# Kernel optimization log

Hardware: AMD Instinct MI355X
Metric: run time of the kernel (lower is better)

## Reference

```python
import math
import jax, jax.numpy as jnp
import numpy as np

L, W, H, T, B = 12, 1024, 16, 1024, 2
CH = W // H  # per-head channels
SCALE = 1.0 / math.sqrt(math.sqrt(CH))
STD = 0.25 * math.sqrt(1.0 / W)  # init_scale * sqrt(1/width)


def setup_inputs() -> dict:
    key = jax.random.key(0)
    ks = jax.random.split(key, 8)
    x = jax.random.normal(ks[0], (B, T, W), dtype=jnp.float32)
    qkv_w = jax.random.normal(ks[1], (L, W, 3 * W), dtype=jnp.float32) * STD
    qkv_b = jnp.zeros((L, 3 * W), jnp.float32)
    proj_w = jax.random.normal(ks[2], (L, W, W), dtype=jnp.float32) * STD
    proj_b = jnp.zeros((L, W), jnp.float32)
    ln1_g = jnp.ones((L, W), jnp.float32)
    ln1_b = jnp.zeros((L, W), jnp.float32)
    ln2_g = jnp.ones((L, W), jnp.float32)
    ln2_b = jnp.zeros((L, W), jnp.float32)
    fc_w = jax.random.normal(ks[3], (L, W, 4 * W), dtype=jnp.float32) * STD
    fc_b = jnp.zeros((L, 4 * W), jnp.float32)
    fc2_w = jax.random.normal(ks[4], (L, 4 * W, W), dtype=jnp.float32) * STD
    fc2_b = jnp.zeros((L, W), jnp.float32)
    return dict(x=x, qkv_w=qkv_w, qkv_b=qkv_b, proj_w=proj_w, proj_b=proj_b,
                ln1_g=ln1_g, ln1_b=ln1_b, ln2_g=ln2_g, ln2_b=ln2_b,
                fc_w=fc_w, fc_b=fc_b, fc2_w=fc2_w, fc2_b=fc2_b)


def _ln(x, g, b, eps=1e-5):
    mu = jnp.mean(x, axis=-1, keepdims=True)
    var = jnp.mean(jnp.square(x - mu), axis=-1, keepdims=True)
    return (x - mu) * jax.lax.rsqrt(var + eps) * g + b


def _attn(h, w_qkv, b_qkv, w_p, b_p):
    bs, t, w = h.shape
    qkv = (h @ w_qkv + b_qkv).reshape(bs, t, H, 3 * CH)
    q, k, v = jnp.split(qkv, 3, axis=-1)  # each [bs, t, H, CH]
    # double-sqrt scaling as in QKVMultiheadAttention
    wts = jnp.einsum('bthc,bshc->bhts', q * SCALE, k * SCALE)
    wts = jax.nn.softmax(wts.astype(jnp.float32), axis=-1).astype(h.dtype)
    o = jnp.einsum('bhts,bshc->bthc', wts, v).reshape(bs, t, w)
    return o @ w_p + b_p


def reference(x, qkv_w, qkv_b, proj_w, proj_b, ln1_g, ln1_b, ln2_g, ln2_b,
              fc_w, fc_b, fc2_w, fc2_b):
    def step(h, p):
        wq, bq, wp, bp, g1, b1, g2, b2, wf, bf, w2, b2m = p
        h = h + _attn(_ln(h, g1, b1), wq, bq, wp, bp)
        z = _ln(h, g2, b2)
        h = h + (jax.nn.gelu(z @ wf + bf, approximate=False) @ w2 + b2m)
        return h, None
    params = (qkv_w, qkv_b, proj_w, proj_b, ln1_g, ln1_b, ln2_g, ln2_b,
              fc_w, fc_b, fc2_w, fc2_b)
    out, _ = jax.lax.scan(step, x, params)
    return out
```

## Files before the change

kernel.cpp:

```cpp
#include <hip/hip_runtime.h>
#include <hip/hip_bf16.h>
#include <math.h>

typedef __bf16 bf16;
typedef __bf16 bf16x8 __attribute__((ext_vector_type(8)));
typedef __bf16 bf16x4 __attribute__((ext_vector_type(4)));
typedef float  f32x4  __attribute__((ext_vector_type(4)));

#define DEV __device__ __forceinline__

DEV void lds_load16(const void* g, void* l) {
  __builtin_amdgcn_global_load_lds(
      (__attribute__((address_space(1))) unsigned int*)g,
      (__attribute__((address_space(3))) unsigned int*)l, 16, 0, 0);
}

DEV f32x4 mfma16(bf16x8 a, bf16x8 b, f32x4 c) {
  return __builtin_amdgcn_mfma_f32_16x16x32_bf16(a, b, c, 0, 0, 0);
}

DEV int xcd_swz(int flat, int nwg) {
  int q = nwg >> 3, r = nwg & 7;
  int xcd = flat & 7, idx = flat >> 3;
  return (xcd < r ? xcd * (q + 1) : r * (q + 1) + (xcd - r) * q) + idx;
}

__global__ __launch_bounds__(256) void transpose_cvt(
    const float* __restrict__ in0, bf16* __restrict__ out0, int R, int C) {
  __shared__ float t[32][33];
  size_t zo = (size_t)blockIdx.z * R * C;
  const float* in = in0 + zo;
  bf16* out = out0 + zo;
  int tx = threadIdx.x, ty = threadIdx.y;
  int c0 = blockIdx.x * 32, r0 = blockIdx.y * 32;
#pragma unroll
  for (int i = 0; i < 4; i++)
    t[ty + i * 8][tx] = in[(size_t)(r0 + ty + i * 8) * C + c0 + tx];
  __syncthreads();
#pragma unroll
  for (int i = 0; i < 4; i++)
    out[(size_t)(c0 + ty + i * 8) * R + r0 + tx] = (bf16)t[tx][ty + i * 8];
}

__global__ __launch_bounds__(256) void ln_fwd(
    const float* __restrict__ x, const float* __restrict__ gw,
    const float* __restrict__ bw, bf16* __restrict__ y,
    float* __restrict__ hout) {
  int row = blockIdx.x, tid = threadIdx.x;
  const float4 v = ((const float4*)(x + (size_t)row * 1024))[tid];
  if (hout) ((float4*)(hout + (size_t)row * 1024))[tid] = v;
  float s  = v.x + v.y + v.z + v.w;
  float s2 = v.x * v.x + v.y * v.y + v.z * v.z + v.w * v.w;
#pragma unroll
  for (int o = 1; o < 64; o <<= 1) {
    s  += __shfl_xor(s, o);
    s2 += __shfl_xor(s2, o);
  }
  __shared__ float ps[4], ps2[4];
  int wv = tid >> 6;
  if ((tid & 63) == 0) { ps[wv] = s; ps2[wv] = s2; }
  __syncthreads();
  s  = ps[0] + ps[1] + ps[2] + ps[3];
  s2 = ps2[0] + ps2[1] + ps2[2] + ps2[3];
  float mu  = s * (1.f / 1024.f);
  float var = s2 * (1.f / 1024.f) - mu * mu;
  float rs  = rsqrtf(var + 1e-5f);
  float4 gv = ((const float4*)gw)[tid];
  float4 bv = ((const float4*)bw)[tid];
  bf16x4 o4;
  o4[0] = (bf16)((v.x - mu) * rs * gv.x + bv.x);
  o4[1] = (bf16)((v.y - mu) * rs * gv.y + bv.y);
  o4[2] = (bf16)((v.z - mu) * rs * gv.z + bv.z);
  o4[3] = (bf16)((v.w - mu) * rs * gv.w + bv.w);
  *(bf16x4*)(y + (size_t)row * 1024 + tid * 4) = o4;
}

__global__ __launch_bounds__(256) void reduce_ln(
    const float* __restrict__ parts, int nparts, const float* __restrict__ bias,
    float* __restrict__ h, const float* __restrict__ gw,
    const float* __restrict__ bw, bf16* __restrict__ y) {
  const int row = blockIdx.x, tid = threadIdx.x;
  const size_t MN = (size_t)gridDim.x * 1024;
  const size_t rb = (size_t)row * 256;
  float4 s = ((const float4*)parts)[rb + tid];
  for (int p = 1; p < nparts; p++) {
    float4 v = ((const float4*)(parts + (size_t)p * MN))[rb + tid];
    s.x += v.x; s.y += v.y; s.z += v.z; s.w += v.w;
  }
  const float4 bb = ((const float4*)bias)[tid];
  float4 r = ((float4*)h)[rb + tid];
  r.x += s.x + bb.x; r.y += s.y + bb.y; r.z += s.z + bb.z; r.w += s.w + bb.w;
  ((float4*)h)[rb + tid] = r;
  if (gw == nullptr) return;
  float sm  = r.x + r.y + r.z + r.w;
  float sm2 = r.x * r.x + r.y * r.y + r.z * r.z + r.w * r.w;
#pragma unroll
  for (int o = 1; o < 64; o <<= 1) {
    sm  += __shfl_xor(sm, o);
    sm2 += __shfl_xor(sm2, o);
  }
  __shared__ float ps[4], ps2[4];
  int wv = tid >> 6;
  if ((tid & 63) == 0) { ps[wv] = sm; ps2[wv] = sm2; }
  __syncthreads();
  sm  = ps[0] + ps[1] + ps[2] + ps[3];
  sm2 = ps2[0] + ps2[1] + ps2[2] + ps2[3];
  float mu  = sm * (1.f / 1024.f);
  float var = sm2 * (1.f / 1024.f) - mu * mu;
  float rs  = rsqrtf(var + 1e-5f);
  float4 gv = ((const float4*)gw)[tid];
  float4 bv = ((const float4*)bw)[tid];
  bf16x4 o4;
  o4[0] = (bf16)((r.x - mu) * rs * gv.x + bv.x);
  o4[1] = (bf16)((r.y - mu) * rs * gv.y + bv.y);
  o4[2] = (bf16)((r.z - mu) * rs * gv.z + bv.z);
  o4[3] = (bf16)((r.w - mu) * rs * gv.w + bv.w);
  *(bf16x4*)(y + (size_t)row * 1024 + tid * 4) = o4;
}

template <int EPI>
__global__ __launch_bounds__(512, 2) void gemm8p(
    const bf16* __restrict__ A, const bf16* __restrict__ Bt,
    const float* __restrict__ bias, float* __restrict__ outf,
    bf16* __restrict__ outb, int M, int N, int K, int kcount) {
  __shared__ __align__(16) char lds[3 * 49152];
  const int tid = threadIdx.x, wv = tid >> 6, lane = tid & 63;
  const int g = lane >> 4, lr = lane & 15;
  const int wr = wv >> 2, wc = wv & 3;
  const int nwg = gridDim.x * gridDim.y;
  const int wgid = xcd_swz(blockIdx.y * gridDim.x + blockIdx.x, nwg);
  const int bn = wgid % gridDim.x, bm = wgid / gridDim.x;
  const int kbegin = blockIdx.z * kcount;
  const bf16* Ab = A + (size_t)bm * 128 * K + kbegin;
  const bf16* Bb = Bt + (size_t)bn * 256 * K + kbegin;
  const int nt = kcount >> 6;

  f32x4 acc[4][4] = {};

  auto stageA = [&](int t) {
    char* dst = lds + (t % 3) * 49152;
    int k0 = t * 64;
#pragma unroll
    for (int c = 0; c < 2; c++) {
      int off = c * 8192 + tid * 16;
      int row = off >> 7, cb = off & 127;
      int cbs = cb ^ ((row & 7) << 4);
      lds_load16((const char*)(Ab + (size_t)row * K + k0) + cbs, dst + off);
    }
  };
  auto stageB = [&](int t, int half) {
    char* dst = lds + (t % 3) * 49152 + 16384 + half * 16384;
    int k0 = t * 64;
#pragma unroll
    for (int c = 0; c < 2; c++) {
      int off = c * 8192 + tid * 16;
      int row = (off >> 7) + half * 128, cb = off & 127;
      int cbs = cb ^ ((row & 7) << 4);
      lds_load16((const char*)(Bb + (size_t)row * K + k0) + cbs, dst + off);
    }
  };
  auto ldA = [&](int t, int m, int kk) -> bf16x8 {
    const char* base = lds + (t % 3) * 49152;
    int row = wr * 64 + m * 16 + lr;
    int col = (kk * 64 + g * 16) ^ ((row & 7) << 4);
    return *(const bf16x8*)(base + row * 128 + col);
  };
  auto ldB = [&](int t, int n, int kk) -> bf16x8 {
    const char* base = lds + (t % 3) * 49152 + 16384;
    int row = wc * 64 + n * 16 + lr;
    int col = (kk * 64 + g * 16) ^ ((row & 7) << 4);
    return *(const bf16x8*)(base + row * 128 + col);
  };

  stageA(0); stageB(0, 0); stageB(0, 1);
  if (nt > 1) {
    stageA(1); stageB(1, 0); stageB(1, 1);
    asm volatile("s_waitcnt vmcnt(6)" ::: "memory");
  } else {
    asm volatile("s_waitcnt vmcnt(0)" ::: "memory");
  }
  __builtin_amdgcn_s_barrier();

  bf16x8 a[4][2], b[4][2];
  for (int t = 0; t < nt; ++t) {
#pragma unroll
    for (int m = 0; m < 4; m++)
#pragma unroll
      for (int kk = 0; kk < 2; kk++) a[m][kk] = ldA(t, m, kk);
#pragma unroll
    for (int n = 0; n < 2; n++)
#pragma unroll
      for (int kk = 0; kk < 2; kk++) b[n][kk] = ldB(t, n, kk);
    if (t + 2 < nt) { stageA(t + 2); stageB(t + 2, 0); }
    __builtin_amdgcn_s_barrier();
    asm volatile("s_waitcnt lgkmcnt(0)" ::: "memory");
    __builtin_amdgcn_sched_barrier(0);
    __builtin_amdgcn_s_setprio(1);
#pragma unroll
    for (int m = 0; m < 4; m++)
#pragma unroll
      for (int n = 0; n < 2; n++)
#pragma unroll
        for (int kk = 0; kk < 2; kk++)
          acc[m][n] = mfma16(a[m][kk], b[n][kk], acc[m][n]);
    __builtin_amdgcn_s_setprio(0);
    __builtin_amdgcn_s_barrier();
#pragma unroll
    for (int n = 2; n < 4; n++)
#pragma unroll
      for (int kk = 0; kk < 2; kk++) b[n][kk] = ldB(t, n, kk);
    if (t + 2 < nt) {
      stageB(t + 2, 1);
      asm volatile("s_waitcnt vmcnt(6)" ::: "memory");
    } else if (t + 1 < nt) {
      asm volatile("s_waitcnt vmcnt(0)" ::: "memory");
    }
    __builtin_amdgcn_s_barrier();
    asm volatile("s_waitcnt lgkmcnt(0)" ::: "memory");
    __builtin_amdgcn_sched_barrier(0);
    __builtin_amdgcn_s_setprio(1);
#pragma unroll
    for (int m = 0; m < 4; m++)
#pragma unroll
      for (int n = 2; n < 4; n++)
#pragma unroll
        for (int kk = 0; kk < 2; kk++)
          acc[m][n] = mfma16(a[m][kk], b[n][kk], acc[m][n]);
    __builtin_amdgcn_s_setprio(0);
    __builtin_amdgcn_s_barrier();
  }

  float* po = (EPI == 3) ? outf + (size_t)blockIdx.z * M * N : outf;
#pragma unroll
  for (int m = 0; m < 4; m++) {
#pragma unroll
    for (int n = 0; n < 4; n++) {
      int col = bn * 256 + wc * 64 + n * 16 + lr;
      float bv = (EPI == 3) ? 0.f : bias[col];
#pragma unroll
      for (int r = 0; r < 4; r++) {
        int row = bm * 128 + wr * 64 + m * 16 + g * 4 + r;
        size_t idx = (size_t)row * N + col;
        float v = acc[m][n][r] + bv;
        if (EPI == 0) {
          outb[idx] = (bf16)v;
        } else if (EPI == 2) {
          outb[idx] = (bf16)(0.5f * v * (1.f + erff(v * 0.70710678118f)));
        } else {
          po[idx] = v;
        }
      }
    }
  }
}

__global__ __launch_bounds__(256) void attn_fwd(
    const bf16* __restrict__ qkv, bf16* __restrict__ outp) {
  __shared__ __align__(16) bf16 Kls[2][128 * 64];
  __shared__ __align__(16) bf16 Vt[2][64 * 128];
  __shared__ __align__(16) bf16 Pls[4 * 16 * 128];
  const int tid = threadIdx.x, wv = tid >> 6, lane = tid & 63;
  const int g = lane >> 4, lr = lane & 15;
  const int wgid = xcd_swz(blockIdx.y * gridDim.x + blockIdx.x,
                           gridDim.x * gridDim.y);
  const int bh = wgid / gridDim.x, bb = bh >> 4, hh = bh & 15;
  const int q0 = (wgid % gridDim.x) * 64;
  const bf16* base = qkv + (size_t)bb * 1024 * 3072;
  const int qc = hh * 192, kc = qc + 64, vc = qc + 128;

  auto kstage = [&](int t, int buf) {
#pragma unroll
    for (int c = 0; c < 4; c++) {
      int off = wv * 4096 + c * 1024 + lane * 16;
      int s = off >> 7, cb = off & 127;
      int cbs = cb ^ ((s & 7) << 4);
      lds_load16(
          (const char*)(base + (size_t)(t * 128 + s) * 3072 + kc) + cbs,
          (char*)Kls[buf] + off);
    }
  };

  bf16x8 aq[2];
  {
    int row = q0 + wv * 16 + lr;
#pragma unroll
    for (int kk = 0; kk < 2; kk++) {
      bf16x8 v = *(const bf16x8*)(base + (size_t)row * 3072 + qc + kk * 32 + g * 8);
#pragma unroll
      for (int j = 0; j < 8; j++) v[j] = (bf16)((float)v[j] * 0.1803368801f);
      aq[kk] = v;
    }
  }

  f32x4 o[4] = {};
  float rm[4], rl[4];
#pragma unroll
  for (int r = 0; r < 4; r++) { rm[r] = -1e30f; rl[r] = 0.f; }

  kstage(0, 0);
#pragma unroll
  for (int it = 0; it < 2; it++) {
    int idx = it * 256 + tid;
    int s = (idx >> 3) * 2, c0i = (idx & 7) * 8;
    bf16x8 v0 = *(const bf16x8*)(base + (size_t)s * 3072 + vc + c0i);
    bf16x8 v1 = *(const bf16x8*)(base + (size_t)(s + 1) * 3072 + vc + c0i);
#pragma unroll
    for (int j = 0; j < 8; j++) {
      int c = c0i + j;
      unsigned int pk = (unsigned int)__builtin_bit_cast(unsigned short, v0[j]) |
                        ((unsigned int)__builtin_bit_cast(unsigned short, v1[j]) << 16);
      *(unsigned int*)((char*)Vt[0] + c * 256 + ((s * 2) ^ ((c & 7) << 4))) = pk;
    }
  }

  for (int ti = 0; ti < 8; ++ti) {
    const int cur = ti & 1, nxt = cur ^ 1;
    __syncthreads();
    f32x4 sa[8] = {};
#pragma unroll
    for (int kk = 0; kk < 2; kk++) {
#pragma unroll
      for (int n = 0; n < 8; n++) {
        int srow = n * 16 + lr;
        int cbyte = (kk * 32 + g * 8) * 2;
        bf16x8 kb = *(const bf16x8*)((char*)Kls[cur] + srow * 128 +
                                     (cbyte ^ ((srow & 7) << 4)));
        sa[n] = mfma16(aq[kk], kb, sa[n]);
      }
    }
    bf16x8 vreg[2][2];
    if (ti + 1 < 8) {
      kstage(ti + 1, nxt);
#pragma unroll
      for (int it = 0; it < 2; it++) {
        int idx = it * 256 + tid;
        int s = (idx >> 3) * 2, c0i = (idx & 7) * 8;
        vreg[it][0] = *(const bf16x8*)(
            base + (size_t)((ti + 1) * 128 + s) * 3072 + vc + c0i);
        vreg[it][1] = *(const bf16x8*)(
            base + (size_t)((ti + 1) * 128 + s + 1) * 3072 + vc + c0i);
      }
    }
    float al[4];
#pragma unroll
    for (int r = 0; r < 4; r++) {
      float tm = -1e30f;
#pragma unroll
      for (int n = 0; n < 8; n++) tm = fmaxf(tm, sa[n][r]);
      tm = fmaxf(tm, __shfl_xor(tm, 1));
      tm = fmaxf(tm, __shfl_xor(tm, 2));
      tm = fmaxf(tm, __shfl_xor(tm, 4));
      tm = fmaxf(tm, __shfl_xor(tm, 8));
      float nm = fmaxf(rm[r], tm);
      al[r] = exp2f(rm[r] - nm);
      rm[r] = nm;
    }
    float psum[4] = {0.f, 0.f, 0.f, 0.f};
#pragma unroll
    for (int n = 0; n < 8; n++) {
#pragma unroll
      for (int r = 0; r < 4; r++) {
        float p = exp2f(sa[n][r] - rm[r]);
        psum[r] += p;
        int rw = g * 4 + r;
        int sb = (n * 16 + lr) * 2;
        *(bf16*)((char*)Pls + wv * 4096 + rw * 256 + (sb ^ ((rw & 7) << 4))) =
            (bf16)p;
      }
    }
#pragma unroll
    for (int r = 0; r < 4; r++) {
      psum[r] += __shfl_xor(psum[r], 1);
      psum[r] += __shfl_xor(psum[r], 2);
      psum[r] += __shfl_xor(psum[r], 4);
      psum[r] += __shfl_xor(psum[r], 8);
      rl[r] = rl[r] * al[r] + psum[r];
#pragma unroll
      for (int n = 0; n < 4; n++) o[n][r] *= al[r];
    }
    asm volatile("s_waitcnt lgkmcnt(0)" ::: "memory");
    __builtin_amdgcn_sched_barrier(0);
#pragma unroll
    for (int sc = 0; sc < 4; sc++) {
      int sb = (sc * 32 + g * 8) * 2;
      bf16x8 pa = *(const bf16x8*)((char*)Pls + wv * 4096 + lr * 256 +
                                   (sb ^ ((lr & 7) << 4)));
#pragma unroll
      for (int n = 0; n < 4; n++) {
        int c = n * 16 + lr;
        bf16x8 vb = *(const bf16x8*)((char*)Vt[cur] + c * 256 +
                                     (sb ^ ((c & 7) << 4)));
        o[n] = mfma16(pa, vb, o[n]);
      }
    }
    if (ti + 1 < 8) {
#pragma unroll
      for (int it = 0; it < 2; it++) {
        int idx = it * 256 + tid;
        int s = (idx >> 3) * 2, c0i = (idx & 7) * 8;
#pragma unroll
        for (int j = 0; j < 8; j++) {
          int c = c0i + j;
          unsigned int pk =
              (unsigned int)__builtin_bit_cast(unsigned short, vreg[it][0][j]) |
              ((unsigned int)__builtin_bit_cast(unsigned short, vreg[it][1][j])
               << 16);
          *(unsigned int*)((char*)Vt[nxt] + c * 256 + ((s * 2) ^ ((c & 7) << 4))) =
              pk;
        }
      }
    }
  }
#pragma unroll
  for (int n = 0; n < 4; n++)
#pragma unroll
    for (int r = 0; r < 4; r++) {
      int row = q0 + wv * 16 + g * 4 + r;
      int col = hh * 64 + n * 16 + lr;
      outp[(size_t)(bb * 1024 + row) * 1024 + col] = (bf16)(o[n][r] / rl[r]);
    }
}

extern "C" void kernel_launch(void* const* d_in, const int* in_sizes, int n_in,
                              void* d_out, int out_size, void* d_ws,
                              size_t ws_size, hipStream_t stream) {
  const float* x      = (const float*)d_in[0];
  const float* qkv_w  = (const float*)d_in[1];
  const float* qkv_b  = (const float*)d_in[2];
  const float* proj_w = (const float*)d_in[3];
  const float* proj_b = (const float*)d_in[4];
  const float* ln1_g  = (const float*)d_in[5];
  const float* ln1_b  = (const float*)d_in[6];
  const float* ln2_g  = (const float*)d_in[7];
  const float* ln2_b  = (const float*)d_in[8];
  const float* fc_w   = (const float*)d_in[9];
  const float* fc_b   = (const float*)d_in[10];
  const float* fc2_w  = (const float*)d_in[11];
  const float* fc2_b  = (const float*)d_in[12];
  float* h = (float*)d_out;

  char* ws = (char*)d_ws;
  size_t off = 0;
  auto alloc = [&](size_t bytes) -> char* {
    char* p = ws + off;
    off = (off + bytes + 255) & ~(size_t)255;
    return p;
  };
  bf16* wq_t    = (bf16*)alloc((size_t)12 * 3072 * 1024 * 2);
  bf16* wp_t    = (bf16*)alloc((size_t)12 * 1024 * 1024 * 2);
  bf16* wf_t    = (bf16*)alloc((size_t)12 * 4096 * 1024 * 2);
  bf16* w2_t    = (bf16*)alloc((size_t)12 * 1024 * 4096 * 2);
  bf16* lnbuf   = (bf16*)alloc((size_t)2048 * 1024 * 2);
  bf16* qkvbuf  = (bf16*)alloc((size_t)2048 * 3072 * 2);
  bf16* attnbuf = (bf16*)alloc((size_t)2048 * 1024 * 2);
  bf16* fcbuf   = (bf16*)alloc((size_t)2048 * 4096 * 2);
  float* partbuf = (float*)alloc((size_t)4 * 2048 * 1024 * 4);

  transpose_cvt<<<dim3(96, 32, 12), dim3(32, 8), 0, stream>>>(qkv_w, wq_t, 1024, 3072);
  transpose_cvt<<<dim3(32, 32, 12), dim3(32, 8), 0, stream>>>(proj_w, wp_t, 1024, 1024);
  transpose_cvt<<<dim3(128, 32, 12), dim3(32, 8), 0, stream>>>(fc_w, wf_t, 1024, 4096);
  transpose_cvt<<<dim3(32, 128, 12), dim3(32, 8), 0, stream>>>(fc2_w, w2_t, 4096, 1024);

  ln_fwd<<<2048, 256, 0, stream>>>(x, ln1_g, ln1_b, lnbuf, h);

  for (int l = 0; l < 12; l++) {
    const bf16* wq = wq_t + (size_t)l * 3072 * 1024;
    const bf16* wp = wp_t + (size_t)l * 1024 * 1024;
    const bf16* wf = wf_t + (size_t)l * 4096 * 1024;
    const bf16* w2 = w2_t + (size_t)l * 1024 * 4096;

    gemm8p<0><<<dim3(12, 16, 1), 512, 0, stream>>>(
        lnbuf, wq, qkv_b + (size_t)l * 3072, nullptr, qkvbuf, 2048, 3072, 1024,
        1024);
    attn_fwd<<<dim3(16, 32), 256, 0, stream>>>(qkvbuf, attnbuf);
    gemm8p<3><<<dim3(4, 16, 4), 512, 0, stream>>>(
        attnbuf, wp, nullptr, partbuf, nullptr, 2048, 1024, 1024, 256);
    reduce_ln<<<2048, 256, 0, stream>>>(partbuf, 4, proj_b + (size_t)l * 1024,
                                        h, ln2_g + (size_t)l * 1024,
                                        ln2_b + (size_t)l * 1024, lnbuf);
    gemm8p<2><<<dim3(16, 16, 1), 512, 0, stream>>>(
        lnbuf, wf, fc_b + (size_t)l * 4096, nullptr, fcbuf, 2048, 4096, 1024,
        1024);
    gemm8p<3><<<dim3(4, 16, 4), 512, 0, stream>>>(
        fcbuf, w2, nullptr, partbuf, nullptr, 2048, 1024, 4096, 1024);
    if (l < 11) {
      reduce_ln<<<2048, 256, 0, stream>>>(
          partbuf, 4, fc2_b + (size_t)l * 1024, h,
          ln1_g + (size_t)(l + 1) * 1024, ln1_b + (size_t)(l + 1) * 1024,
          lnbuf);
    } else {
      reduce_ln<<<2048, 256, 0, stream>>>(partbuf, 4,
                                          fc2_b + (size_t)l * 1024, h, nullptr,
                                          nullptr, nullptr);
    }
  }
}
```

Measured before the change: 1.838 ms.

## Widen weight transpose tiles with vector IO and add lazy softmax rescaling

The weight transpose-convert kernel now works on 64x64 tiles, reading rows with float4 loads and writing sixteen bf16 values per thread as two 16-byte stores, which cuts the number of narrow global transactions when converting all layer weights each call. The flash-attention online softmax also skips updating the running max and rescaling the accumulator unless the new max exceeds the old one by more than a threshold in the log2 domain. That removes exp2 and multiply work per tile but lets un-normalised values grow by up to 2^11 before rescaling, which risks precision loss in bf16 P values. The column-strided LDS reads in the transpose may cause bank conflicts.

```diff
diff --git a/kernel.cpp b/kernel.cpp
--- a/kernel.cpp
+++ b/kernel.cpp
@@ -27,19 +27,30 @@
 
 __global__ __launch_bounds__(256) void transpose_cvt(
     const float* __restrict__ in0, bf16* __restrict__ out0, int R, int C) {
-  __shared__ float t[32][33];
+  __shared__ float t[64][65];
   size_t zo = (size_t)blockIdx.z * R * C;
   const float* in = in0 + zo;
   bf16* out = out0 + zo;
-  int tx = threadIdx.x, ty = threadIdx.y;
-  int c0 = blockIdx.x * 32, r0 = blockIdx.y * 32;
-#pragma unroll
-  for (int i = 0; i < 4; i++)
-    t[ty + i * 8][tx] = in[(size_t)(r0 + ty + i * 8) * C + c0 + tx];
+  int c0 = blockIdx.x * 64, r0 = blockIdx.y * 64;
+  int tr = threadIdx.x >> 4, tc4 = (threadIdx.x & 15) * 4;
+#pragma unroll
+  for (int i = 0; i < 4; i++) {
+    float4 v = *(const float4*)(in + (size_t)(r0 + tr + i * 16) * C + c0 + tc4);
+    t[tr + i * 16][tc4 + 0] = v.x;
+    t[tr + i * 16][tc4 + 1] = v.y;
+    t[tr + i * 16][tc4 + 2] = v.z;
+    t[tr + i * 16][tc4 + 3] = v.w;
+  }
   __syncthreads();
-#pragma unroll
-  for (int i = 0; i < 4; i++)
-    out[(size_t)(c0 + ty + i * 8) * R + r0 + tx] = (bf16)t[tx][ty + i * 8];
+  int oc = threadIdx.x >> 2, j = threadIdx.x & 3;
+  bf16x8 o0, o1;
+#pragma unroll
+  for (int i = 0; i < 8; i++) o0[i] = (bf16)t[j * 16 + i][oc];
+#pragma unroll
+  for (int i = 0; i < 8; i++) o1[i] = (bf16)t[j * 16 + 8 + i][oc];
+  bf16* op = out + (size_t)(c0 + oc) * R + r0 + j * 16;
+  *(bf16x8*)op = o0;
+  *(bf16x8*)(op + 8) = o1;
 }
 
 __global__ __launch_bounds__(256) void ln_fwd(
@@ -351,9 +362,12 @@
       tm = fmaxf(tm, __shfl_xor(tm, 2));
       tm = fmaxf(tm, __shfl_xor(tm, 4));
       tm = fmaxf(tm, __shfl_xor(tm, 8));
-      float nm = fmaxf(rm[r], tm);
-      al[r] = exp2f(rm[r] - nm);
-      rm[r] = nm;
+      if (tm - rm[r] <= 11.0f) {
+        al[r] = 1.0f;
+      } else {
+        al[r] = exp2f(rm[r] - tm);
+        rm[r] = tm;
+      }
     }
     float psum[4] = {0.f, 0.f, 0.f, 0.f};
 #pragma unroll
@@ -375,8 +389,10 @@
       psum[r] += __shfl_xor(psum[r], 4);
       psum[r] += __shfl_xor(psum[r], 8);
       rl[r] = rl[r] * al[r] + psum[r];
-#pragma unroll
-      for (int n = 0; n < 4; n++) o[n][r] *= al[r];
+      if (al[r] != 1.0f) {
+#pragma unroll
+        for (int n = 0; n < 4; n++) o[n][r] *= al[r];
+      }
     }
     asm volatile("s_waitcnt lgkmcnt(0)" ::: "memory");
     __builtin_amdgcn_sched_barrier(0);
@@ -456,10 +472,10 @@
   bf16* fcbuf   = (bf16*)alloc((size_t)2048 * 4096 * 2);
   float* partbuf = (float*)alloc((size_t)4 * 2048 * 1024 * 4);
 
-  transpose_cvt<<<dim3(96, 32, 12), dim3(32, 8), 0, stream>>>(qkv_w, wq_t, 1024, 3072);
-  transpose_cvt<<<dim3(32, 32, 12), dim3(32, 8), 0, stream>>>(proj_w, wp_t, 1024, 1024);
-  transpose_cvt<<<dim3(128, 32, 12), dim3(32, 8), 0, stream>>>(fc_w, wf_t, 1024, 4096);
-  transpose_cvt<<<dim3(32, 128, 12), dim3(32, 8), 0, stream>>>(fc2_w, w2_t, 4096, 1024);
+  transpose_cvt<<<dim3(48, 16, 12), 256, 0, stream>>>(qkv_w, wq_t, 1024, 3072);
+  transpose_cvt<<<dim3(16, 16, 12), 256, 0, stream>>>(proj_w, wp_t, 1024, 1024);
+  transpose_cvt<<<dim3(64, 16, 12), 256, 0, stream>>>(fc_w, wf_t, 1024, 4096);
+  transpose_cvt<<<dim3(16, 64, 12), 256, 0, stream>>>(fc2_w, w2_t, 4096, 1024);
 
   ln_fwd<<<2048, 256, 0, stream>>>(x, ln1_g, ln1_b, lnbuf, h);
 
```

After: 1.843 ms. Within noise of the previous version (+0.2%).
